# Performance work log

Measured on AMD Instinct MI355X. Metric: run time of the kernel, lower is better.

Reference implementation:

```python
import jax, jax.numpy as jnp
import numpy as np

B, S, IN, OUT = 4, 2048, 4096, 4096

def setup_inputs() -> dict:
    key = jax.random.key(0)
    k1, k2, k3, k4 = jax.random.split(key, 4)
    input = jax.random.normal(k1, (B, S, IN), dtype=jnp.float32)
    # int8-valued weights stored as int32 (range [-128, 127])
    weight_int8 = jax.random.randint(k2, (OUT, IN), -128, 128, dtype=jnp.int32)
    scale = jax.random.uniform(k3, (OUT, 1), dtype=jnp.float32, minval=0.001, maxval=0.02)
    zero_point = jnp.zeros((OUT, 1), dtype=jnp.float32)
    bias = jax.random.normal(k4, (OUT,), dtype=jnp.float32)
    return {"input": input, "weight_int8": weight_int8, "scale": scale,
            "zero_point": zero_point, "bias": bias}

def reference(input, weight_int8, scale, zero_point, bias):
    # Dequantize: per-output-channel affine (w - zp) * s, then linear.
    w = (weight_int8.astype(input.dtype) - zero_point) * scale  # [OUT, IN]
    out = jnp.einsum('bsi,oi->bso', input, w)
    return out + bias
```

## Files before the change

### kernel.cpp

```cpp
#include <hip/hip_runtime.h>
#include <cstdint>
#include <cstddef>


#define BM 128
#define BN 128
#define BK 32

typedef __bf16 bf16x8 __attribute__((ext_vector_type(8)));
typedef float floatx4 __attribute__((ext_vector_type(4)));
typedef float float4v __attribute__((ext_vector_type(4)));
typedef int int4v __attribute__((ext_vector_type(4)));
typedef unsigned short ushort8v __attribute__((ext_vector_type(8)));
typedef unsigned short ushort4v __attribute__((ext_vector_type(4)));

#define AS1 __attribute__((address_space(1)))
#define AS3 __attribute__((address_space(3)))

__device__ __forceinline__ void load16_g2l(const void* g, void* l) {
    __builtin_amdgcn_global_load_lds((const AS1 void*)(uintptr_t)g,
                                     (AS3 void*)(uint32_t)(uintptr_t)l,
                                     16, 0, 0);
}

__device__ __forceinline__ unsigned short f2bf(float f) {
    union { float f; uint32_t u; } v; v.f = f;
    uint32_t u = v.u;
    uint32_t r = (u + 0x7fffu + ((u >> 16) & 1u)) >> 16;
    return (unsigned short)r;
}

__global__ __launch_bounds__(256) void cvt_f32_bf16(
    const float* __restrict__ in, unsigned short* __restrict__ out, int n) {
    int i = (blockIdx.x * 256 + threadIdx.x) * 8;
    if (i + 8 > n) {
        for (; i < n; ++i) out[i] = f2bf(in[i]);
        return;
    }
    float4v f0 = *(const float4v*)(in + i);
    float4v f1 = *(const float4v*)(in + i + 4);
    ushort8v r;
    r[0] = f2bf(f0[0]); r[1] = f2bf(f0[1]); r[2] = f2bf(f0[2]); r[3] = f2bf(f0[3]);
    r[4] = f2bf(f1[0]); r[5] = f2bf(f1[1]); r[6] = f2bf(f1[2]); r[7] = f2bf(f1[3]);
    *(ushort8v*)(out + i) = r;
}

__global__ __launch_bounds__(256) void dequant_w(
    const int* __restrict__ w, const float* __restrict__ scale,
    const float* __restrict__ zp, unsigned short* __restrict__ out, int K) {
    const int row = blockIdx.x;
    const float s = scale[row];
    const float z = zp[row];
    const size_t base = (size_t)row * K;
    for (int c = threadIdx.x * 4; c < K; c += 256 * 4) {
        int4v wv = *(const int4v*)(w + base + c);
        ushort4v o;
        o[0] = f2bf(((float)wv[0] - z) * s);
        o[1] = f2bf(((float)wv[1] - z) * s);
        o[2] = f2bf(((float)wv[2] - z) * s);
        o[3] = f2bf(((float)wv[3] - z) * s);
        *(ushort4v*)(out + base + c) = o;
    }
}

__global__ __launch_bounds__(256) void gemm_bf16_bt(
    const unsigned short* __restrict__ A,
    const unsigned short* __restrict__ B,
    const float* __restrict__ bias,
    float* __restrict__ C,
    int M, int N, int K) {
    __shared__ unsigned short lds_a[BM * BK];
    __shared__ unsigned short lds_b[BN * BK];

    const int tid = threadIdx.x;
    const int lane = tid & 63;
    const int wave = tid >> 6;

    const int n0 = blockIdx.x * BN;
    const int m0 = blockIdx.y * BM;

    const int wm = (wave >> 1) * 64;
    const int wn = (wave & 1) * 64;

    floatx4 acc[4][4];
    const floatx4 zero = {0.f, 0.f, 0.f, 0.f};
#pragma unroll
    for (int i = 0; i < 4; ++i)
#pragma unroll
        for (int j = 0; j < 4; ++j) acc[i][j] = zero;

    const int fl0 = tid, fl1 = tid + 256;
    const int row0 = fl0 >> 2, row1 = fl1 >> 2;
    const int kc0 = (fl0 & 3) * 8, kc1 = (fl1 & 3) * 8;

    const unsigned short* ga0 = A + (size_t)(m0 + row0) * K + kc0;
    const unsigned short* ga1 = A + (size_t)(m0 + row1) * K + kc1;
    const unsigned short* gb0 = B + (size_t)(n0 + row0) * K + kc0;
    const unsigned short* gb1 = B + (size_t)(n0 + row1) * K + kc1;

    unsigned short* la0 = &lds_a[fl0 * 8];
    unsigned short* la1 = &lds_a[fl1 * 8];
    unsigned short* lb0 = &lds_b[fl0 * 8];
    unsigned short* lb1 = &lds_b[fl1 * 8];

    const int fm = lane & 15;
    const int fq = lane >> 4;

    const unsigned short* ra[4];
    const unsigned short* rb[4];
#pragma unroll
    for (int t = 0; t < 4; ++t) {
        ra[t] = &lds_a[(wm + t * 16 + fm) * BK + fq * 8];
        rb[t] = &lds_b[(wn + t * 16 + fm) * BK + fq * 8];
    }

    for (int k0 = 0; k0 < K; k0 += BK) {
        __syncthreads();
        load16_g2l(ga0 + k0, la0);
        load16_g2l(ga1 + k0, la1);
        load16_g2l(gb0 + k0, lb0);
        load16_g2l(gb1 + k0, lb1);
        __syncthreads();

        bf16x8 av[4], bv[4];
#pragma unroll
        for (int t = 0; t < 4; ++t) av[t] = *(const bf16x8*)ra[t];
#pragma unroll
        for (int t = 0; t < 4; ++t) bv[t] = *(const bf16x8*)rb[t];
#pragma unroll
        for (int i = 0; i < 4; ++i)
#pragma unroll
            for (int j = 0; j < 4; ++j)
                acc[i][j] = __builtin_amdgcn_mfma_f32_16x16x32_bf16(
                    av[i], bv[j], acc[i][j], 0, 0, 0);
    }

#pragma unroll
    for (int j = 0; j < 4; ++j) {
        const int col = n0 + wn + j * 16 + fm;
        const float bvl = bias[col];
#pragma unroll
        for (int i = 0; i < 4; ++i) {
            const int rbase = m0 + wm + i * 16 + fq * 4;
#pragma unroll
            for (int r = 0; r < 4; ++r) {
                C[(size_t)(rbase + r) * N + col] = acc[i][j][r] + bvl;
            }
        }
    }
}

__global__ __launch_bounds__(256) void fallback_naive(
    const float* __restrict__ in, const int* __restrict__ w,
    const float* __restrict__ scale, const float* __restrict__ zp,
    const float* __restrict__ bias, float* __restrict__ out,
    int M, int N, int K) {
    int idx = blockIdx.x * 256 + threadIdx.x;
    if (idx >= M * N) return;
    int m = idx / N, n = idx - m * N;
    const float s = scale[n], z = zp[n];
    const float* a = in + (size_t)m * K;
    const int* wr = w + (size_t)n * K;
    float acc = 0.f;
    for (int k = 0; k < K; ++k) acc += a[k] * ((float)wr[k] - z);
    out[idx] = acc * s + bias[n];
}

extern "C" void kernel_launch(void* const* d_in, const int* in_sizes, int n_in,
                              void* d_out, int out_size, void* d_ws, size_t ws_size,
                              hipStream_t stream) {
    constexpr int M = 4 * 2048;
    constexpr int K = 4096;
    constexpr int N = 4096;

    const float* input = (const float*)d_in[0];
    const int* w8 = (const int*)d_in[1];
    const float* scale = (const float*)d_in[2];
    const float* zp = (const float*)d_in[3];
    const float* bias = (const float*)d_in[4];
    float* out = (float*)d_out;

    const size_t need = ((size_t)M * K + (size_t)N * K) * sizeof(unsigned short);
    if (ws_size < need) {
        const int total = M * N;
        fallback_naive<<<(total + 255) / 256, 256, 0, stream>>>(
            input, w8, scale, zp, bias, out, M, N, K);
        return;
    }

    unsigned short* wsA = (unsigned short*)d_ws;
    unsigned short* wsW = wsA + (size_t)M * K;

    const int nA = M * K;
    cvt_f32_bf16<<<nA / (256 * 8), 256, 0, stream>>>(input, wsA, nA);
    dequant_w<<<N, 256, 0, stream>>>(w8, scale, zp, wsW, K);

    dim3 grid(N / BN, M / BM);
    gemm_bf16_bt<<<grid, 256, 0, stream>>>(wsA, wsW, bias, out, M, N, K);
}
```

Baseline: 610.1 us.

## Fuse conversion kernels into one launch and XOR-swizzle LDS tiles

The separate activation-conversion and weight-dequant kernels become a single prep kernel that splits its grid between the two jobs, dropping one launch and letting both run concurrently. The GEMM's LDS layout gets an XOR swizzle of the 16-byte k-chunk index by row, applied on both the global-to-LDS write side and the MFMA fragment read side, to cut LDS bank conflicts on the fragment reads. The prep kernel's row computation hardcodes K=4096 through a shift.

```diff
diff --git a/kernel.cpp b/kernel.cpp
--- a/kernel.cpp
+++ b/kernel.cpp
@@ -30,36 +30,30 @@
     return (unsigned short)r;
 }
 
-__global__ __launch_bounds__(256) void cvt_f32_bf16(
-    const float* __restrict__ in, unsigned short* __restrict__ out, int n) {
-    int i = (blockIdx.x * 256 + threadIdx.x) * 8;
-    if (i + 8 > n) {
-        for (; i < n; ++i) out[i] = f2bf(in[i]);
-        return;
-    }
-    float4v f0 = *(const float4v*)(in + i);
-    float4v f1 = *(const float4v*)(in + i + 4);
-    ushort8v r;
-    r[0] = f2bf(f0[0]); r[1] = f2bf(f0[1]); r[2] = f2bf(f0[2]); r[3] = f2bf(f0[3]);
-    r[4] = f2bf(f1[0]); r[5] = f2bf(f1[1]); r[6] = f2bf(f1[2]); r[7] = f2bf(f1[3]);
-    *(ushort8v*)(out + i) = r;
-}
-
-__global__ __launch_bounds__(256) void dequant_w(
+__global__ __launch_bounds__(256) void prep(
+    const float* __restrict__ a_in, unsigned short* __restrict__ a_out,
     const int* __restrict__ w, const float* __restrict__ scale,
-    const float* __restrict__ zp, unsigned short* __restrict__ out, int K) {
-    const int row = blockIdx.x;
-    const float s = scale[row];
-    const float z = zp[row];
-    const size_t base = (size_t)row * K;
-    for (int c = threadIdx.x * 4; c < K; c += 256 * 4) {
-        int4v wv = *(const int4v*)(w + base + c);
+    const float* __restrict__ zp, unsigned short* __restrict__ w_out,
+    int ga_blocks) {
+    const int bid = blockIdx.x;
+    if (bid < ga_blocks) {
+        const size_t i = ((size_t)bid * 256 + threadIdx.x) * 4;
+        float4v f = *(const float4v*)(a_in + i);
+        ushort4v r;
+        r[0] = f2bf(f[0]); r[1] = f2bf(f[1]); r[2] = f2bf(f[2]); r[3] = f2bf(f[3]);
+        *(ushort4v*)(a_out + i) = r;
+    } else {
+        const size_t i = ((size_t)(bid - ga_blocks) * 256 + threadIdx.x) * 4;
+        const int row = (int)(i >> 12);
+        const float s = scale[row];
+        const float z = zp[row];
+        int4v wv = *(const int4v*)(w + i);
         ushort4v o;
         o[0] = f2bf(((float)wv[0] - z) * s);
         o[1] = f2bf(((float)wv[1] - z) * s);
         o[2] = f2bf(((float)wv[2] - z) * s);
         o[3] = f2bf(((float)wv[3] - z) * s);
-        *(ushort4v*)(out + base + c) = o;
+        *(ushort4v*)(w_out + i) = o;
     }
 }
 
@@ -91,7 +85,8 @@
 
     const int fl0 = tid, fl1 = tid + 256;
     const int row0 = fl0 >> 2, row1 = fl1 >> 2;
-    const int kc0 = (fl0 & 3) * 8, kc1 = (fl1 & 3) * 8;
+    const int kc0 = (((fl0 & 3) ^ ((row0 >> 1) & 3)) * 8);
+    const int kc1 = (((fl1 & 3) ^ ((row1 >> 1) & 3)) * 8);
 
     const unsigned short* ga0 = A + (size_t)(m0 + row0) * K + kc0;
     const unsigned short* ga1 = A + (size_t)(m0 + row1) * K + kc1;
@@ -105,13 +100,16 @@
 
     const int fm = lane & 15;
     const int fq = lane >> 4;
+    const int swz = fq ^ ((fm >> 1) & 3);
 
     const unsigned short* ra[4];
     const unsigned short* rb[4];
 #pragma unroll
     for (int t = 0; t < 4; ++t) {
-        ra[t] = &lds_a[(wm + t * 16 + fm) * BK + fq * 8];
-        rb[t] = &lds_b[(wn + t * 16 + fm) * BK + fq * 8];
+        const int pa = (wm + t * 16 + fm) * 4 + swz;
+        const int pb = (wn + t * 16 + fm) * 4 + swz;
+        ra[t] = &lds_a[pa * 8];
+        rb[t] = &lds_b[pb * 8];
     }
 
     for (int k0 = 0; k0 < K; k0 += BK) {
@@ -191,9 +189,10 @@
     unsigned short* wsA = (unsigned short*)d_ws;
     unsigned short* wsW = wsA + (size_t)M * K;
 
-    const int nA = M * K;
-    cvt_f32_bf16<<<nA / (256 * 8), 256, 0, stream>>>(input, wsA, nA);
-    dequant_w<<<N, 256, 0, stream>>>(w8, scale, zp, wsW, K);
+    const int ga_blocks = (M * K) / 1024;
+    const int gw_blocks = (N * K) / 1024;
+    prep<<<ga_blocks + gw_blocks, 256, 0, stream>>>(
+        input, wsA, w8, scale, zp, wsW, ga_blocks);
 
     dim3 grid(N / BN, M / BM);
     gemm_bf16_bt<<<grid, 256, 0, stream>>>(wsA, wsW, bias, out, M, N, K);
```

New measurement: 589.3 us. 3.4% less time.
